# Kernel optimization log

Measured on AMD Instinct MI355X. Metric: run time of the kernel, lower is better.

The kernel has to match this reference:

```python
import jax, jax.numpy as jnp
import numpy as np

DIMS = 1024
STATE = 2 * DIMS
EPS = 1e-8


def _rmsnorm(v, scale):
    # norm = ||v||_2 * d^{-1/2}
    d = v.shape[-1]
    n = jnp.sqrt(jnp.sum(v * v, axis=-1, keepdims=True)) * (d ** -0.5)
    return scale * v / (n + EPS)


def setup_inputs() -> dict:
    key = jax.random.key(0)
    ks = jax.random.split(key, 5)
    x = jax.random.normal(ks[0], (4, 2048, DIMS), dtype=jnp.float32)
    ls_scale = jnp.ones((DIMS // 2,), dtype=jnp.float32)
    rs_scale = jnp.ones((DIMS // 2,), dtype=jnp.float32)
    split_scale = jnp.full((DIMS,), 0.1, dtype=jnp.float32)
    sk = (1.0 / DIMS) ** 0.5
    Wk = jax.random.uniform(ks[1], (DIMS, STATE), jnp.float32, -sk, sk)
    Wugg = jax.random.uniform(ks[2], (DIMS, 3 * STATE), jnp.float32, -sk, sk)
    so = (1.0 / STATE) ** 0.5
    Wout = jax.random.uniform(ks[3], (STATE, DIMS), jnp.float32, -so, so)
    return {"x": x, "ls_scale": ls_scale, "rs_scale": rs_scale,
            "split_scale": split_scale, "Wk": Wk, "Wugg": Wugg, "Wout": Wout}


def reference(x, ls_scale, rs_scale, split_scale, Wk, Wugg, Wout):
    residual = x
    # RMS_split norm (output_dim=None)
    xl, xr = jnp.split(x, 2, axis=-1)
    xn = jnp.concatenate([_rmsnorm(xl, ls_scale), _rmsnorm(xr, rs_scale)], axis=-1)
    xn = xn * split_scale

    K = jax.nn.sigmoid(xn @ Wk)                      # [B,S,STATE]
    u, g_in, g_out = jnp.split(xn @ Wugg, 3, axis=-1)
    u = u * jax.nn.sigmoid(g_in) * (1.0 - K)

    # linear recurrence: h_0 = u_0; h_t = K_{t-1} * h_{t-1} + u_t
    a = jnp.concatenate([jnp.ones_like(K[..., :1, :]), K[..., :-1, :]], axis=-2)

    def combine(lhs, rhs):
        aL, bL = lhs
        aR, bR = rhs
        return (aL * aR, bL * aR + bR)

    _, h = jax.lax.associative_scan(combine, (a, u), axis=1)
    outputs = h * jax.nn.sigmoid(g_out)
    y = outputs @ Wout
    return y + residual
```

## Files before the change

### kernel.cpp

```cpp
#include <hip/hip_runtime.h>
#include <hip/hip_bf16.h>
#include <hip/hip_fp8.h>
#include <stdint.h>

#define DIMS 1024
#define STATE 2048
#define BATCH 4
#define SEQ 2048
#define TOKENS 8192
#define N1 8192
#define NCHUNK 16
#define CHUNKL (SEQ / NCHUNK)

typedef __hip_bfloat16 bf16;
typedef unsigned char u8;
typedef unsigned short u16;
typedef __attribute__((ext_vector_type(8))) short bf16x8;
typedef __attribute__((ext_vector_type(4))) float f32x4;
typedef __attribute__((ext_vector_type(16))) float f32x16;
typedef __attribute__((ext_vector_type(2))) long v2i64;

#define XN_SCALE 32.0f
#define W1_SCALE 256.0f
#define INV_SCALE (1.0f / 8192.0f)

__device__ __forceinline__ float sigmoidf_(float x) {
  return 1.0f / (1.0f + __expf(-x));
}

__device__ __forceinline__ u8 to_fp8(float f) {
  __hip_fp8_e4m3 h(f);
  return h.__x;
}

__device__ __forceinline__ float b2f(u16 v) {
  union { uint32_t u; float f; } w;
  w.u = ((uint32_t)v) << 16;
  return w.f;
}

__device__ __forceinline__ int kperm(int k) {
  return (k & ~24) | ((k & 8) << 1) | ((k & 16) >> 1);
}

__device__ __forceinline__ void async_copy16(const void* g, void* l) {
  __builtin_amdgcn_global_load_lds(
      (const __attribute__((address_space(1))) void*)(uintptr_t)g,
      (__attribute__((address_space(3))) void*)(uint32_t)(uintptr_t)l,
      16, 0, 0);
}

__device__ __forceinline__ int swz32(int row, int kc) {
  int line = row >> 1;
  int sub = ((row & 1) << 2) | kc;
  return (line << 3) | (sub ^ (line & 7));
}
__device__ __forceinline__ void swz32_dec(int c, int& row, int& kc) {
  int line = c >> 3;
  int sub = (c & 7) ^ (line & 7);
  row = (line << 1) | (sub >> 2);
  kc = sub & 3;
}
__device__ __forceinline__ int swz64(int row, int kc) {
  return (row << 3) | (kc ^ (row & 7));
}
__device__ __forceinline__ void swz64_dec(int c, int& row, int& kc) {
  row = c >> 3;
  kc = (c & 7) ^ (row & 7);
}

__global__ __launch_bounds__(256) void transpose_bf16_kernel(
    const float* __restrict__ W, bf16* __restrict__ Wt, int K, int N) {
  __shared__ float tile[32][33];
  int tx = threadIdx.x & 31;
  int ty = threadIdx.x >> 5;
  long col = (long)blockIdx.x * 32 + tx;
  long rowb = (long)blockIdx.y * 32;
#pragma unroll
  for (int i = 0; i < 32; i += 8)
    tile[ty + i][tx] = W[(rowb + ty + i) * N + col];
  __syncthreads();
  long ocol = rowb + tx;
  long orow = (long)blockIdx.x * 32 + ty;
#pragma unroll
  for (int i = 0; i < 32; i += 8)
    Wt[(orow + i) * K + ocol] = __float2bfloat16(tile[tx][ty + i]);
}

__global__ __launch_bounds__(256) void transpose_fp8_kernel(
    const float* __restrict__ W, u8* __restrict__ Wt, int K, int N, int stream_base) {
  __shared__ float tile[32][33];
  int tx = threadIdx.x & 31;
  int ty = threadIdx.x >> 5;
  long col = (long)blockIdx.x * 32 + tx;
  long rowb = (long)blockIdx.y * 32;
#pragma unroll
  for (int i = 0; i < 32; i += 8)
    tile[ty + i][tx] = W[(rowb + ty + i) * N + col];
  __syncthreads();
  long ocol = rowb + kperm(tx);
  long orow = (long)blockIdx.x * 32 + ty;
#pragma unroll
  for (int i = 0; i < 32; i += 8) {
    long n = orow + i;
    long dstrow = ((n & 2047) << 2) | (stream_base + (n >> 11));
    Wt[dstrow * K + ocol] = to_fp8(tile[tx][ty + i] * W1_SCALE);
  }
}

__global__ __launch_bounds__(256) void rmsnorm_kernel(
    const float* __restrict__ x, const float* __restrict__ ls,
    const float* __restrict__ rs, const float* __restrict__ ss,
    u8* __restrict__ xn8) {
  int token = blockIdx.x;
  int tid = threadIdx.x;
  const float4* xt = (const float4*)(x + (long)token * DIMS);
  float4 v = xt[tid];
  float s = v.x * v.x + v.y * v.y + v.z * v.z + v.w * v.w;
#pragma unroll
  for (int d = 32; d > 0; d >>= 1) s += __shfl_down(s, d);
  __shared__ float parts[4];
  if ((tid & 63) == 0) parts[tid >> 6] = s;
  __syncthreads();
  int j = tid * 4;
  bool left = j < 512;
  float sum = left ? (parts[0] + parts[1]) : (parts[2] + parts[3]);
  float n = sqrtf(sum * (1.0f / 512.0f));
  float inv = 1.0f / (n + 1e-8f);
  const float4* sc = (const float4*)(left ? ls : rs);
  float4 g = sc[left ? tid : tid - 128];
  float4 p = ((const float4*)ss)[tid];
  u8 q[4];
  q[0] = to_fp8(v.x * g.x * inv * p.x * XN_SCALE);
  q[1] = to_fp8(v.y * g.y * inv * p.y * XN_SCALE);
  q[2] = to_fp8(v.z * g.z * inv * p.z * XN_SCALE);
  q[3] = to_fp8(v.w * g.w * inv * p.w * XN_SCALE);
  *(uint32_t*)(xn8 + (long)token * DIMS + kperm(j)) = *(uint32_t*)q;
}

__device__ __forceinline__ void g1f8_stage(const u8* __restrict__ A,
                                           const u8* __restrict__ Bt,
                                           long arow0, long brow0, int k0,
                                           int wave, int lane, u8* As, u8* Bs) {
  const int K = DIMS;
#pragma unroll
  for (int i = 0; i < 4; i++) {
    int c = (wave * 4 + i) * 64 + lane;
    int row, kc; swz32_dec(c, row, kc);
    async_copy16(A + (arow0 + row) * K + k0 + kc * 16, (char*)As + (wave * 4 + i) * 1024);
  }
#pragma unroll
  for (int i = 0; i < 2; i++) {
    int c = (wave * 2 + i) * 64 + lane;
    int row, kc; swz32_dec(c, row, kc);
    async_copy16(Bt + (brow0 + row) * K + k0 + kc * 16, (char*)Bs + (wave * 2 + i) * 1024);
  }
}

__global__ __launch_bounds__(256, 2) void gemm1_fp8(
    const u8* __restrict__ A, const u8* __restrict__ Bt, bf16* __restrict__ C) {
  __shared__ __align__(16) u8 As0[256 * 64], As1[256 * 64];
  __shared__ __align__(16) u8 Bs0[128 * 64], Bs1[128 * 64];
  int tid = threadIdx.x;
  int lane = tid & 63, wave = tid >> 6;
  int wm = wave & 1, wn = wave >> 1;
  long arow0 = (long)blockIdx.y * 256;
  long brow0 = (long)blockIdx.x * 128;
  int m_lane = lane & 31, q4 = lane >> 5;
  f32x16 acc[4][2] = {};

  g1f8_stage(A, Bt, arow0, brow0, 0, wave, lane, As0, Bs0);
  __syncthreads();

  for (int it = 0; it < 16; it += 2) {
    {
      v2i64 af[2][4], bfr[2][2];
#pragma unroll
      for (int p = 0; p < 2; p++) {
#pragma unroll
        for (int mt = 0; mt < 4; mt++)
          af[p][mt] = *(const v2i64*)(As0 + swz32(wm * 128 + mt * 32 + m_lane, p * 2 + q4) * 16);
#pragma unroll
        for (int nt = 0; nt < 2; nt++)
          bfr[p][nt] = *(const v2i64*)(Bs0 + swz32(wn * 64 + nt * 32 + m_lane, p * 2 + q4) * 16);
      }
      g1f8_stage(A, Bt, arow0, brow0, (it + 1) * 64, wave, lane, As1, Bs1);
#pragma unroll
      for (int p = 0; p < 2; p++)
#pragma unroll
        for (int mt = 0; mt < 4; mt++)
#pragma unroll
          for (int nt = 0; nt < 2; nt++) {
            acc[mt][nt] = __builtin_amdgcn_mfma_f32_32x32x16_fp8_fp8(bfr[p][nt][0], af[p][mt][0], acc[mt][nt], 0, 0, 0);
            acc[mt][nt] = __builtin_amdgcn_mfma_f32_32x32x16_fp8_fp8(bfr[p][nt][1], af[p][mt][1], acc[mt][nt], 0, 0, 0);
          }
      __syncthreads();
    }
    {
      v2i64 af[2][4], bfr[2][2];
#pragma unroll
      for (int p = 0; p < 2; p++) {
#pragma unroll
        for (int mt = 0; mt < 4; mt++)
          af[p][mt] = *(const v2i64*)(As1 + swz32(wm * 128 + mt * 32 + m_lane, p * 2 + q4) * 16);
#pragma unroll
        for (int nt = 0; nt < 2; nt++)
          bfr[p][nt] = *(const v2i64*)(Bs1 + swz32(wn * 64 + nt * 32 + m_lane, p * 2 + q4) * 16);
      }
      if (it + 2 < 16)
        g1f8_stage(A, Bt, arow0, brow0, (it + 2) * 64, wave, lane, As0, Bs0);
#pragma unroll
      for (int p = 0; p < 2; p++)
#pragma unroll
        for (int mt = 0; mt < 4; mt++)
#pragma unroll
          for (int nt = 0; nt < 2; nt++) {
            acc[mt][nt] = __builtin_amdgcn_mfma_f32_32x32x16_fp8_fp8(bfr[p][nt][0], af[p][mt][0], acc[mt][nt], 0, 0, 0);
            acc[mt][nt] = __builtin_amdgcn_mfma_f32_32x32x16_fp8_fp8(bfr[p][nt][1], af[p][mt][1], acc[mt][nt], 0, 0, 0);
          }
      __syncthreads();
    }
  }
#pragma unroll
  for (int mt = 0; mt < 4; mt++) {
    long row = arow0 + wm * 128 + mt * 32 + m_lane;
#pragma unroll
    for (int nt = 0; nt < 2; nt++) {
#pragma unroll
      for (int g = 0; g < 4; g++) {
        long col = brow0 + wn * 64 + nt * 32 + g * 8 + q4 * 4;
        bf16 tmp[4];
#pragma unroll
        for (int j = 0; j < 4; j++)
          tmp[j] = __float2bfloat16(acc[mt][nt][g * 4 + j] * INV_SCALE);
        *(uint2*)(C + row * N1 + col) = *(uint2*)tmp;
      }
    }
  }
}

__device__ __forceinline__ void g2_stage(const bf16* __restrict__ A,
                                         const bf16* __restrict__ Bt,
                                         long arow0, long brow0, int k0, int K,
                                         int wave, int lane, bf16* As, bf16* Bs) {
#pragma unroll
  for (int i = 0; i < 4; i++) {
    int c = (wave * 4 + i) * 64 + lane;
    int row, kc; swz64_dec(c, row, kc);
    async_copy16(A + (arow0 + row) * K + k0 + kc * 8, (char*)As + (wave * 4 + i) * 1024);
    async_copy16(Bt + (brow0 + row) * K + k0 + kc * 8, (char*)Bs + (wave * 4 + i) * 1024);
  }
}

__global__ __launch_bounds__(256) void gemm2_resid(
    const bf16* __restrict__ A, const bf16* __restrict__ Bt,
    float* __restrict__ C, const float* __restrict__ resid) {
  __shared__ __align__(16) bf16 As0[128 * 64], As1[128 * 64];
  __shared__ __align__(16) bf16 Bs0[128 * 64], Bs1[128 * 64];
  const int K = STATE, N = DIMS;
  int tid = threadIdx.x;
  int lane = tid & 63, wave = tid >> 6;
  int wm = wave & 1, wn = wave >> 1;
  long arow0 = (long)blockIdx.y * 128;
  long brow0 = (long)blockIdx.x * 128;
  int r = lane & 15, q = lane >> 4;
  f32x4 acc[4][4] = {};

  g2_stage(A, Bt, arow0, brow0, 0, K, wave, lane, As0, Bs0);
  __syncthreads();

  for (int it = 0; it < 32; it += 2) {
    {
      const bf16x8* AsV = (const bf16x8*)As0;
      const bf16x8* BsV = (const bf16x8*)Bs0;
      bf16x8 af[2][4], bfr[2][4];
#pragma unroll
      for (int ks = 0; ks < 2; ks++) {
#pragma unroll
        for (int mt = 0; mt < 4; mt++) af[ks][mt] = AsV[swz64(wm * 64 + mt * 16 + r, ks * 4 + q)];
#pragma unroll
        for (int nt = 0; nt < 4; nt++) bfr[ks][nt] = BsV[swz64(wn * 64 + nt * 16 + r, ks * 4 + q)];
      }
      g2_stage(A, Bt, arow0, brow0, (it + 1) * 64, K, wave, lane, As1, Bs1);
#pragma unroll
      for (int ks = 0; ks < 2; ks++)
#pragma unroll
        for (int mt = 0; mt < 4; mt++)
#pragma unroll
          for (int nt = 0; nt < 4; nt++)
            acc[mt][nt] = __builtin_amdgcn_mfma_f32_16x16x32_bf16(bfr[ks][nt], af[ks][mt], acc[mt][nt], 0, 0, 0);
      __syncthreads();
    }
    {
      const bf16x8* AsV = (const bf16x8*)As1;
      const bf16x8* BsV = (const bf16x8*)Bs1;
      bf16x8 af[2][4], bfr[2][4];
#pragma unroll
      for (int ks = 0; ks < 2; ks++) {
#pragma unroll
        for (int mt = 0; mt < 4; mt++) af[ks][mt] = AsV[swz64(wm * 64 + mt * 16 + r, ks * 4 + q)];
#pragma unroll
        for (int nt = 0; nt < 4; nt++) bfr[ks][nt] = BsV[swz64(wn * 64 + nt * 16 + r, ks * 4 + q)];
      }
      if (it + 2 < 32)
        g2_stage(A, Bt, arow0, brow0, (it + 2) * 64, K, wave, lane, As0, Bs0);
#pragma unroll
      for (int ks = 0; ks < 2; ks++)
#pragma unroll
        for (int mt = 0; mt < 4; mt++)
#pragma unroll
          for (int nt = 0; nt < 4; nt++)
            acc[mt][nt] = __builtin_amdgcn_mfma_f32_16x16x32_bf16(bfr[ks][nt], af[ks][mt], acc[mt][nt], 0, 0, 0);
      __syncthreads();
    }
  }

#pragma unroll
  for (int mt = 0; mt < 4; mt++) {
    long row = arow0 + wm * 64 + mt * 16 + r;
#pragma unroll
    for (int nt = 0; nt < 4; nt++) {
      long col = brow0 + wn * 64 + nt * 16 + q * 4;
      float4 rv = *(const float4*)(resid + row * N + col);
      float4 ov;
      ov.x = acc[mt][nt][0] + rv.x;
      ov.y = acc[mt][nt][1] + rv.y;
      ov.z = acc[mt][nt][2] + rv.z;
      ov.w = acc[mt][nt][3] + rv.w;
      *(float4*)(C + row * N + col) = ov;
    }
  }
}


__global__ __launch_bounds__(256) void chunk_summary_kernel(
    const bf16* __restrict__ C1, float* __restrict__ carryA,
    float* __restrict__ carryU) {
  int b = blockIdx.x;
  int ch = blockIdx.y * 256 + threadIdx.x;
  int chunk = blockIdx.z;
  int t0 = chunk * CHUNKL;
  const bf16* base = C1 + ((long)b * SEQ) * N1 + ch * 4;
  float kp = 0.0f;
  if (chunk != 0) kp = __bfloat162float(base[(long)(t0 - 1) * N1]);
  float a_first = (chunk == 0) ? 1.0f : sigmoidf_(kp);
  float A = 1.0f, U = 0.0f;
#pragma unroll 8
  for (int t = t0; t < t0 + CHUNKL; t++) {
    union { uint2 u2; u16 h[4]; } w;
    w.u2 = *(const uint2*)(base + (long)t * N1);
    float kraw = b2f(w.h[0]);
    float uraw = b2f(w.h[1]);
    float gin  = b2f(w.h[2]);
    float a = (t == t0) ? a_first : sigmoidf_(kp);
    float sK = sigmoidf_(kraw);
    float u = uraw * sigmoidf_(gin) * (1.0f - sK);
    A *= a;
    U = a * U + u;
    kp = kraw;
  }
  int cidx = (b * NCHUNK + chunk) * STATE + ch;
  carryA[cidx] = A;
  carryU[cidx] = U;
}

__global__ __launch_bounds__(256) void carry_scan_kernel(
    const float* __restrict__ carryA, const float* __restrict__ carryU,
    float* __restrict__ carryIn) {
  int idx = blockIdx.x * 256 + threadIdx.x;
  int b = idx >> 11;
  int ch = idx & 2047;
  float h = 0.0f;
#pragma unroll
  for (int c = 0; c < NCHUNK; c++) {
    int cidx = (b * NCHUNK + c) * STATE + ch;
    carryIn[cidx] = h;
    h = carryA[cidx] * h + carryU[cidx];
  }
}

__global__ __launch_bounds__(256) void scan_chunk_kernel(
    const bf16* __restrict__ C1, const float* __restrict__ carryIn,
    bf16* __restrict__ out) {
  int b = blockIdx.x;
  int c0 = blockIdx.y * 32;
  int chunk = blockIdx.z;
  int tstart = chunk * CHUNKL;
  __shared__ float a_s[32][65], u_s[32][65], h_s[32][65];
  int tid = threadIdx.x;
  int lane = tid & 63, wave = tid >> 6;
  int cc = tid & 31;
  int tq = tid >> 5;

  float carryH[8], carryK[8];
#pragma unroll
  for (int i = 0; i < 8; i++) {
    int ch = c0 + wave * 8 + i;
    carryH[i] = carryIn[(b * NCHUNK + chunk) * STATE + ch];
    carryK[i] = (chunk == 0)
                    ? 1.0f
                    : sigmoidf_(__bfloat162float(
                          C1[((long)(b * SEQ + tstart - 1)) * N1 + ch * 4]));
  }

  float g_r[8];
  for (int t0 = tstart; t0 < tstart + CHUNKL; t0 += 64) {
#pragma unroll
    for (int i = 0; i < 8; i++) {
      int t = tq * 8 + i;
      union { uint2 u2; u16 h[4]; } w;
      w.u2 = *(const uint2*)(C1 + ((long)(b * SEQ + t0 + t)) * N1 + (c0 + cc) * 4);
      float kraw = b2f(w.h[0]);
      float uraw = b2f(w.h[1]);
      float gin  = b2f(w.h[2]);
      float gout = b2f(w.h[3]);
      float aK = sigmoidf_(kraw);
      a_s[cc][t] = aK;
      u_s[cc][t] = uraw * sigmoidf_(gin) * (1.0f - aK);
      g_r[i] = sigmoidf_(gout);
    }
    __syncthreads();
#pragma unroll
    for (int i = 0; i < 8; i++) {
      int ch = wave * 8 + i;
      float aK = a_s[ch][lane];
      float u = u_s[ch][lane];
      float a = __shfl_up(aK, 1);
      if (lane == 0) a = carryK[i];
      float A = a, U = u;
#pragma unroll
      for (int d = 1; d < 64; d <<= 1) {
        float Au = __shfl_up(A, d);
        float Uu = __shfl_up(U, d);
        if (lane >= d) { U += A * Uu; A *= Au; }
      }
      float h = U + A * carryH[i];
      carryH[i] = __shfl(h, 63);
      carryK[i] = __shfl(aK, 63);
      h_s[ch][lane] = h;
    }
    __syncthreads();
#pragma unroll
    for (int i = 0; i < 8; i++) {
      int t = tq * 8 + i;
      out[((long)(b * SEQ + t0 + t)) * STATE + c0 + cc] =
          __float2bfloat16(h_s[cc][t] * g_r[i]);
    }
    __syncthreads();
  }
}

extern "C" void kernel_launch(void* const* d_in, const int* in_sizes, int n_in,
                              void* d_out, int out_size, void* d_ws, size_t ws_size,
                              hipStream_t stream) {
  const float* x    = (const float*)d_in[0];
  const float* ls   = (const float*)d_in[1];
  const float* rs   = (const float*)d_in[2];
  const float* ss   = (const float*)d_in[3];
  const float* Wk   = (const float*)d_in[4];
  const float* Wugg = (const float*)d_in[5];
  const float* Wout = (const float*)d_in[6];
  float* out = (float*)d_out;

  char* ws = (char*)d_ws;
  u8*   W1f8 = (u8*)ws;
  bf16* W2t  = (bf16*)(ws + 8388608);
  u8*   xn8  = (u8*)(ws + 8388608 + 4194304);
  bf16* C1   = (bf16*)(ws + 8388608 + 4194304 + 8388608);
  bf16* sco  = (bf16*)(ws + 8388608 + 4194304 + 8388608 + 134217728);
  float* carryA  = (float*)xn8;
  float* carryU  = carryA + BATCH * NCHUNK * STATE;
  float* carryIn = carryU + BATCH * NCHUNK * STATE;

  transpose_fp8_kernel<<<dim3(STATE / 32, DIMS / 32), 256, 0, stream>>>(
      Wk, W1f8, DIMS, STATE, 0);
  transpose_fp8_kernel<<<dim3(3 * STATE / 32, DIMS / 32), 256, 0, stream>>>(
      Wugg, W1f8, DIMS, 3 * STATE, 1);
  transpose_bf16_kernel<<<dim3(DIMS / 32, STATE / 32), 256, 0, stream>>>(Wout, W2t, STATE, DIMS);

  rmsnorm_kernel<<<TOKENS, 256, 0, stream>>>(x, ls, rs, ss, xn8);

  gemm1_fp8<<<dim3(N1 / 128, TOKENS / 256), 256, 0, stream>>>(xn8, W1f8, C1);

  chunk_summary_kernel<<<dim3(BATCH, STATE / 256, NCHUNK), 256, 0, stream>>>(
      C1, carryA, carryU);
  carry_scan_kernel<<<dim3(BATCH * STATE / 256), 256, 0, stream>>>(
      carryA, carryU, carryIn);
  scan_chunk_kernel<<<dim3(BATCH, STATE / 32, NCHUNK), 256, 0, stream>>>(
      C1, carryIn, sco);

  gemm2_resid<<<dim3(DIMS / 128, TOKENS / 128), 256, 0, stream>>>(
      sco, W2t, out, x);
}
```

Baseline: 387.3 us.

## Fuse gate sigmoids into GEMM1 epilogue, emit packed (a,u) and gate tensors

Moves the sigmoid and gating math out of the scan kernels into the GEMM1 epilogue. GEMM1 now writes a packed bf16 pair (sigmoid(K), u) as one 32-bit word per channel plus a separate bf16 sigmoid(g_out) array, instead of four raw bf16 projections. The summary kernel reads only the packed word, dropping the g_out bytes and the repeated sigmoid work. The total intermediate size stays about the same, but the scan kernels now issue narrower loads from differently strided arrays, and the epilogue stores become 4-byte and 2-byte scattered writes.

```diff
diff --git a/kernel.cpp b/kernel.cpp
--- a/kernel.cpp
+++ b/kernel.cpp
@@ -37,6 +37,11 @@
   union { uint32_t u; float f; } w;
   w.u = ((uint32_t)v) << 16;
   return w.f;
+}
+__device__ __forceinline__ u16 f2bb(float f) {
+  union { bf16 b; u16 u; } v;
+  v.b = __float2bfloat16(f);
+  return v.u;
 }
 
 __device__ __forceinline__ int kperm(int k) {
@@ -158,7 +163,8 @@
 }
 
 __global__ __launch_bounds__(256, 2) void gemm1_fp8(
-    const u8* __restrict__ A, const u8* __restrict__ Bt, bf16* __restrict__ C) {
+    const u8* __restrict__ A, const u8* __restrict__ Bt,
+    uint32_t* __restrict__ P, bf16* __restrict__ G) {
   __shared__ __align__(16) u8 As0[256 * 64], As1[256 * 64];
   __shared__ __align__(16) u8 Bs0[128 * 64], Bs1[128 * 64];
   int tid = threadIdx.x;
@@ -228,12 +234,16 @@
     for (int nt = 0; nt < 2; nt++) {
 #pragma unroll
       for (int g = 0; g < 4; g++) {
-        long col = brow0 + wn * 64 + nt * 32 + g * 8 + q4 * 4;
-        bf16 tmp[4];
-#pragma unroll
-        for (int j = 0; j < 4; j++)
-          tmp[j] = __float2bfloat16(acc[mt][nt][g * 4 + j] * INV_SCALE);
-        *(uint2*)(C + row * N1 + col) = *(uint2*)tmp;
+        long ch = (brow0 >> 2) + wn * 16 + nt * 8 + g * 2 + q4;
+        float kraw = acc[mt][nt][g * 4 + 0] * INV_SCALE;
+        float uraw = acc[mt][nt][g * 4 + 1] * INV_SCALE;
+        float gin  = acc[mt][nt][g * 4 + 2] * INV_SCALE;
+        float gout = acc[mt][nt][g * 4 + 3] * INV_SCALE;
+        float aK = sigmoidf_(kraw);
+        float u  = uraw * sigmoidf_(gin) * (1.0f - aK);
+        float gg = sigmoidf_(gout);
+        P[row * STATE + ch] = (uint32_t)f2bb(aK) | ((uint32_t)f2bb(u) << 16);
+        G[row * STATE + ch] = __float2bfloat16(gg);
       }
     }
   }
@@ -334,30 +344,24 @@
 
 
 __global__ __launch_bounds__(256) void chunk_summary_kernel(
-    const bf16* __restrict__ C1, float* __restrict__ carryA,
+    const uint32_t* __restrict__ P, float* __restrict__ carryA,
     float* __restrict__ carryU) {
   int b = blockIdx.x;
   int ch = blockIdx.y * 256 + threadIdx.x;
   int chunk = blockIdx.z;
   int t0 = chunk * CHUNKL;
-  const bf16* base = C1 + ((long)b * SEQ) * N1 + ch * 4;
-  float kp = 0.0f;
-  if (chunk != 0) kp = __bfloat162float(base[(long)(t0 - 1) * N1]);
-  float a_first = (chunk == 0) ? 1.0f : sigmoidf_(kp);
+  const uint32_t* base = P + ((long)b * SEQ) * STATE + ch;
+  float a_carry = 1.0f;
+  if (chunk != 0) a_carry = b2f((u16)(base[(long)(t0 - 1) * STATE] & 0xffff));
   float A = 1.0f, U = 0.0f;
 #pragma unroll 8
   for (int t = t0; t < t0 + CHUNKL; t++) {
-    union { uint2 u2; u16 h[4]; } w;
-    w.u2 = *(const uint2*)(base + (long)t * N1);
-    float kraw = b2f(w.h[0]);
-    float uraw = b2f(w.h[1]);
-    float gin  = b2f(w.h[2]);
-    float a = (t == t0) ? a_first : sigmoidf_(kp);
-    float sK = sigmoidf_(kraw);
-    float u = uraw * sigmoidf_(gin) * (1.0f - sK);
-    A *= a;
-    U = a * U + u;
-    kp = kraw;
+    uint32_t w = base[(long)t * STATE];
+    float aK = b2f((u16)(w & 0xffff));
+    float u  = b2f((u16)(w >> 16));
+    A *= a_carry;
+    U = a_carry * U + u;
+    a_carry = aK;
   }
   int cidx = (b * NCHUNK + chunk) * STATE + ch;
   carryA[cidx] = A;
@@ -380,8 +384,8 @@
 }
 
 __global__ __launch_bounds__(256) void scan_chunk_kernel(
-    const bf16* __restrict__ C1, const float* __restrict__ carryIn,
-    bf16* __restrict__ out) {
+    const uint32_t* __restrict__ P, const bf16* __restrict__ G,
+    const float* __restrict__ carryIn, bf16* __restrict__ out) {
   int b = blockIdx.x;
   int c0 = blockIdx.y * 32;
   int chunk = blockIdx.z;
@@ -399,8 +403,7 @@
     carryH[i] = carryIn[(b * NCHUNK + chunk) * STATE + ch];
     carryK[i] = (chunk == 0)
                     ? 1.0f
-                    : sigmoidf_(__bfloat162float(
-                          C1[((long)(b * SEQ + tstart - 1)) * N1 + ch * 4]));
+                    : b2f((u16)(P[((long)(b * SEQ + tstart - 1)) * STATE + ch] & 0xffff));
   }
 
   float g_r[8];
@@ -408,16 +411,11 @@
 #pragma unroll
     for (int i = 0; i < 8; i++) {
       int t = tq * 8 + i;
-      union { uint2 u2; u16 h[4]; } w;
-      w.u2 = *(const uint2*)(C1 + ((long)(b * SEQ + t0 + t)) * N1 + (c0 + cc) * 4);
-      float kraw = b2f(w.h[0]);
-      float uraw = b2f(w.h[1]);
-      float gin  = b2f(w.h[2]);
-      float gout = b2f(w.h[3]);
-      float aK = sigmoidf_(kraw);
-      a_s[cc][t] = aK;
-      u_s[cc][t] = uraw * sigmoidf_(gin) * (1.0f - aK);
-      g_r[i] = sigmoidf_(gout);
+      long idx = ((long)(b * SEQ + t0 + t)) * STATE + c0 + cc;
+      uint32_t w = P[idx];
+      a_s[cc][t] = b2f((u16)(w & 0xffff));
+      u_s[cc][t] = b2f((u16)(w >> 16));
+      g_r[i] = __bfloat162float(G[idx]);
     }
     __syncthreads();
 #pragma unroll
@@ -463,11 +461,12 @@
   float* out = (float*)d_out;
 
   char* ws = (char*)d_ws;
-  u8*   W1f8 = (u8*)ws;
-  bf16* W2t  = (bf16*)(ws + 8388608);
-  u8*   xn8  = (u8*)(ws + 8388608 + 4194304);
-  bf16* C1   = (bf16*)(ws + 8388608 + 4194304 + 8388608);
-  bf16* sco  = (bf16*)(ws + 8388608 + 4194304 + 8388608 + 134217728);
+  u8*       W1f8 = (u8*)ws;
+  bf16*     W2t  = (bf16*)(ws + 8388608);
+  u8*       xn8  = (u8*)(ws + 8388608 + 4194304);
+  uint32_t* P    = (uint32_t*)(ws + 20971520);
+  bf16*     G    = (bf16*)(ws + 20971520 + 67108864);
+  bf16*     sco  = (bf16*)(ws + 20971520 + 67108864 + 33554432);
   float* carryA  = (float*)xn8;
   float* carryU  = carryA + BATCH * NCHUNK * STATE;
   float* carryIn = carryU + BATCH * NCHUNK * STATE;
@@ -480,14 +479,14 @@
 
   rmsnorm_kernel<<<TOKENS, 256, 0, stream>>>(x, ls, rs, ss, xn8);
 
-  gemm1_fp8<<<dim3(N1 / 128, TOKENS / 256), 256, 0, stream>>>(xn8, W1f8, C1);
+  gemm1_fp8<<<dim3(N1 / 128, TOKENS / 256), 256, 0, stream>>>(xn8, W1f8, P, G);
 
   chunk_summary_kernel<<<dim3(BATCH, STATE / 256, NCHUNK), 256, 0, stream>>>(
-      C1, carryA, carryU);
+      P, carryA, carryU);
   carry_scan_kernel<<<dim3(BATCH * STATE / 256), 256, 0, stream>>>(
       carryA, carryU, carryIn);
   scan_chunk_kernel<<<dim3(BATCH, STATE / 32, NCHUNK), 256, 0, stream>>>(
-      C1, carryIn, sco);
+      P, G, carryIn, sco);
 
   gemm2_resid<<<dim3(DIMS / 128, TOKENS / 128), 256, 0, stream>>>(
       sco, W2t, out, x);
```

Result: slower. 405.0 us (+4.6%).

## Switch output GEMM to FP8 with scaled scan output and FP8 transposed weights

Applied to the files above, without the earlier changes.

Converts the second GEMM (scan outputs times Wout) from bf16 to fp8 e4m3. The scan kernel now writes fp8 with a fixed scale and k-permuted columns, and the weight transpose emits fp8. The GEMM uses 32x32x16 fp8 MFMAs and rescales in the epilogue. This halves the operand bytes and raises MFMA throughput, at the cost of accuracy risk from fixed-scale fp8 quantization of activations and weights.

```diff
diff --git a/kernel.cpp b/kernel.cpp
--- a/kernel.cpp
+++ b/kernel.cpp
@@ -15,13 +15,14 @@
 typedef __hip_bfloat16 bf16;
 typedef unsigned char u8;
 typedef unsigned short u16;
-typedef __attribute__((ext_vector_type(8))) short bf16x8;
 typedef __attribute__((ext_vector_type(4))) float f32x4;
 typedef __attribute__((ext_vector_type(16))) float f32x16;
 typedef __attribute__((ext_vector_type(2))) long v2i64;
 
 #define XN_SCALE 32.0f
 #define W1_SCALE 256.0f
+#define H_SCALE  32.0f
+#define W2_SCALE 256.0f
 #define INV_SCALE (1.0f / 8192.0f)
 
 __device__ __forceinline__ float sigmoidf_(float x) {
@@ -61,16 +62,10 @@
   row = (line << 1) | (sub >> 2);
   kc = sub & 3;
 }
-__device__ __forceinline__ int swz64(int row, int kc) {
-  return (row << 3) | (kc ^ (row & 7));
-}
-__device__ __forceinline__ void swz64_dec(int c, int& row, int& kc) {
-  row = c >> 3;
-  kc = (c & 7) ^ (row & 7);
-}
-
-__global__ __launch_bounds__(256) void transpose_bf16_kernel(
-    const float* __restrict__ W, bf16* __restrict__ Wt, int K, int N) {
+
+__global__ __launch_bounds__(256) void transpose_fp8_kernel(
+    const float* __restrict__ W, u8* __restrict__ Wt, int K, int N,
+    int stream_base, int interleave, float scale) {
   __shared__ float tile[32][33];
   int tx = threadIdx.x & 31;
   int ty = threadIdx.x >> 5;
@@ -80,31 +75,13 @@
   for (int i = 0; i < 32; i += 8)
     tile[ty + i][tx] = W[(rowb + ty + i) * N + col];
   __syncthreads();
-  long ocol = rowb + tx;
-  long orow = (long)blockIdx.x * 32 + ty;
-#pragma unroll
-  for (int i = 0; i < 32; i += 8)
-    Wt[(orow + i) * K + ocol] = __float2bfloat16(tile[tx][ty + i]);
-}
-
-__global__ __launch_bounds__(256) void transpose_fp8_kernel(
-    const float* __restrict__ W, u8* __restrict__ Wt, int K, int N, int stream_base) {
-  __shared__ float tile[32][33];
-  int tx = threadIdx.x & 31;
-  int ty = threadIdx.x >> 5;
-  long col = (long)blockIdx.x * 32 + tx;
-  long rowb = (long)blockIdx.y * 32;
-#pragma unroll
-  for (int i = 0; i < 32; i += 8)
-    tile[ty + i][tx] = W[(rowb + ty + i) * N + col];
-  __syncthreads();
   long ocol = rowb + kperm(tx);
   long orow = (long)blockIdx.x * 32 + ty;
 #pragma unroll
   for (int i = 0; i < 32; i += 8) {
     long n = orow + i;
-    long dstrow = ((n & 2047) << 2) | (stream_base + (n >> 11));
-    Wt[dstrow * K + ocol] = to_fp8(tile[tx][ty + i] * W1_SCALE);
+    long dstrow = interleave ? (((n & 2047) << 2) | (stream_base + (n >> 11))) : n;
+    Wt[dstrow * K + ocol] = to_fp8(tile[tx][ty + i] * scale);
   }
 }
 
@@ -239,99 +216,109 @@
   }
 }
 
-__device__ __forceinline__ void g2_stage(const bf16* __restrict__ A,
-                                         const bf16* __restrict__ Bt,
-                                         long arow0, long brow0, int k0, int K,
-                                         int wave, int lane, bf16* As, bf16* Bs) {
-#pragma unroll
-  for (int i = 0; i < 4; i++) {
-    int c = (wave * 4 + i) * 64 + lane;
-    int row, kc; swz64_dec(c, row, kc);
-    async_copy16(A + (arow0 + row) * K + k0 + kc * 8, (char*)As + (wave * 4 + i) * 1024);
-    async_copy16(Bt + (brow0 + row) * K + k0 + kc * 8, (char*)Bs + (wave * 4 + i) * 1024);
-  }
-}
-
-__global__ __launch_bounds__(256) void gemm2_resid(
-    const bf16* __restrict__ A, const bf16* __restrict__ Bt,
+__device__ __forceinline__ void g2f8_stage(const u8* __restrict__ A,
+                                           const u8* __restrict__ Bt,
+                                           long arow0, long brow0, int k0,
+                                           int wave, int lane, u8* As, u8* Bs) {
+  const int K = STATE;
+#pragma unroll
+  for (int i = 0; i < 2; i++) {
+    int c = (wave * 2 + i) * 64 + lane;
+    int row, kc; swz32_dec(c, row, kc);
+    async_copy16(A + (arow0 + row) * K + k0 + kc * 16, (char*)As + (wave * 2 + i) * 1024);
+  }
+#pragma unroll
+  for (int i = 0; i < 2; i++) {
+    int c = (wave * 2 + i) * 64 + lane;
+    int row, kc; swz32_dec(c, row, kc);
+    async_copy16(Bt + (brow0 + row) * K + k0 + kc * 16, (char*)Bs + (wave * 2 + i) * 1024);
+  }
+}
+
+__global__ __launch_bounds__(256) void gemm2_fp8(
+    const u8* __restrict__ A, const u8* __restrict__ Bt,
     float* __restrict__ C, const float* __restrict__ resid) {
-  __shared__ __align__(16) bf16 As0[128 * 64], As1[128 * 64];
-  __shared__ __align__(16) bf16 Bs0[128 * 64], Bs1[128 * 64];
-  const int K = STATE, N = DIMS;
+  __shared__ __align__(16) u8 As0[128 * 64], As1[128 * 64];
+  __shared__ __align__(16) u8 Bs0[128 * 64], Bs1[128 * 64];
   int tid = threadIdx.x;
   int lane = tid & 63, wave = tid >> 6;
   int wm = wave & 1, wn = wave >> 1;
   long arow0 = (long)blockIdx.y * 128;
   long brow0 = (long)blockIdx.x * 128;
-  int r = lane & 15, q = lane >> 4;
-  f32x4 acc[4][4] = {};
-
-  g2_stage(A, Bt, arow0, brow0, 0, K, wave, lane, As0, Bs0);
+  int m_lane = lane & 31, q4 = lane >> 5;
+  f32x16 acc[2][2] = {};
+
+  g2f8_stage(A, Bt, arow0, brow0, 0, wave, lane, As0, Bs0);
   __syncthreads();
 
   for (int it = 0; it < 32; it += 2) {
     {
-      const bf16x8* AsV = (const bf16x8*)As0;
-      const bf16x8* BsV = (const bf16x8*)Bs0;
-      bf16x8 af[2][4], bfr[2][4];
-#pragma unroll
-      for (int ks = 0; ks < 2; ks++) {
-#pragma unroll
-        for (int mt = 0; mt < 4; mt++) af[ks][mt] = AsV[swz64(wm * 64 + mt * 16 + r, ks * 4 + q)];
-#pragma unroll
-        for (int nt = 0; nt < 4; nt++) bfr[ks][nt] = BsV[swz64(wn * 64 + nt * 16 + r, ks * 4 + q)];
-      }
-      g2_stage(A, Bt, arow0, brow0, (it + 1) * 64, K, wave, lane, As1, Bs1);
-#pragma unroll
-      for (int ks = 0; ks < 2; ks++)
-#pragma unroll
-        for (int mt = 0; mt < 4; mt++)
-#pragma unroll
-          for (int nt = 0; nt < 4; nt++)
-            acc[mt][nt] = __builtin_amdgcn_mfma_f32_16x16x32_bf16(bfr[ks][nt], af[ks][mt], acc[mt][nt], 0, 0, 0);
+      v2i64 af[2][2], bfr[2][2];
+#pragma unroll
+      for (int p = 0; p < 2; p++) {
+#pragma unroll
+        for (int mt = 0; mt < 2; mt++)
+          af[p][mt] = *(const v2i64*)(As0 + swz32(wm * 64 + mt * 32 + m_lane, p * 2 + q4) * 16);
+#pragma unroll
+        for (int nt = 0; nt < 2; nt++)
+          bfr[p][nt] = *(const v2i64*)(Bs0 + swz32(wn * 64 + nt * 32 + m_lane, p * 2 + q4) * 16);
+      }
+      g2f8_stage(A, Bt, arow0, brow0, (it + 1) * 64, wave, lane, As1, Bs1);
+#pragma unroll
+      for (int p = 0; p < 2; p++)
+#pragma unroll
+        for (int mt = 0; mt < 2; mt++)
+#pragma unroll
+          for (int nt = 0; nt < 2; nt++) {
+            acc[mt][nt] = __builtin_amdgcn_mfma_f32_32x32x16_fp8_fp8(bfr[p][nt][0], af[p][mt][0], acc[mt][nt], 0, 0, 0);
+            acc[mt][nt] = __builtin_amdgcn_mfma_f32_32x32x16_fp8_fp8(bfr[p][nt][1], af[p][mt][1], acc[mt][nt], 0, 0, 0);
+          }
       __syncthreads();
     }
     {
-      const bf16x8* AsV = (const bf16x8*)As1;
-      const bf16x8* BsV = (const bf16x8*)Bs1;
-      bf16x8 af[2][4], bfr[2][4];
-#pragma unroll
-      for (int ks = 0; ks < 2; ks++) {
-#pragma unroll
-        for (int mt = 0; mt < 4; mt++) af[ks][mt] = AsV[swz64(wm * 64 + mt * 16 + r, ks * 4 + q)];
-#pragma unroll
-        for (int nt = 0; nt < 4; nt++) bfr[ks][nt] = BsV[swz64(wn * 64 + nt * 16 + r, ks * 4 + q)];
+      v2i64 af[2][2], bfr[2][2];
+#pragma unroll
+      for (int p = 0; p < 2; p++) {
+#pragma unroll
+        for (int mt = 0; mt < 2; mt++)
+          af[p][mt] = *(const v2i64*)(As1 + swz32(wm * 64 + mt * 32 + m_lane, p * 2 + q4) * 16);
+#pragma unroll
+        for (int nt = 0; nt < 2; nt++)
+          bfr[p][nt] = *(const v2i64*)(Bs1 + swz32(wn * 64 + nt * 32 + m_lane, p * 2 + q4) * 16);
       }
       if (it + 2 < 32)
-        g2_stage(A, Bt, arow0, brow0, (it + 2) * 64, K, wave, lane, As0, Bs0);
-#pragma unroll
-      for (int ks = 0; ks < 2; ks++)
-#pragma unroll
-        for (int mt = 0; mt < 4; mt++)
-#pragma unroll
-          for (int nt = 0; nt < 4; nt++)
-            acc[mt][nt] = __builtin_amdgcn_mfma_f32_16x16x32_bf16(bfr[ks][nt], af[ks][mt], acc[mt][nt], 0, 0, 0);
+        g2f8_stage(A, Bt, arow0, brow0, (it + 2) * 64, wave, lane, As0, Bs0);
+#pragma unroll
+      for (int p = 0; p < 2; p++)
+#pragma unroll
+        for (int mt = 0; mt < 2; mt++)
+#pragma unroll
+          for (int nt = 0; nt < 2; nt++) {
+            acc[mt][nt] = __builtin_amdgcn_mfma_f32_32x32x16_fp8_fp8(bfr[p][nt][0], af[p][mt][0], acc[mt][nt], 0, 0, 0);
+            acc[mt][nt] = __builtin_amdgcn_mfma_f32_32x32x16_fp8_fp8(bfr[p][nt][1], af[p][mt][1], acc[mt][nt], 0, 0, 0);
+          }
       __syncthreads();
     }
   }
-
-#pragma unroll
-  for (int mt = 0; mt < 4; mt++) {
-    long row = arow0 + wm * 64 + mt * 16 + r;
-#pragma unroll
-    for (int nt = 0; nt < 4; nt++) {
-      long col = brow0 + wn * 64 + nt * 16 + q * 4;
-      float4 rv = *(const float4*)(resid + row * N + col);
-      float4 ov;
-      ov.x = acc[mt][nt][0] + rv.x;
-      ov.y = acc[mt][nt][1] + rv.y;
-      ov.z = acc[mt][nt][2] + rv.z;
-      ov.w = acc[mt][nt][3] + rv.w;
-      *(float4*)(C + row * N + col) = ov;
-    }
-  }
-}
-
+#pragma unroll
+  for (int mt = 0; mt < 2; mt++) {
+    long row = arow0 + wm * 64 + mt * 32 + m_lane;
+#pragma unroll
+    for (int nt = 0; nt < 2; nt++) {
+#pragma unroll
+      for (int g = 0; g < 4; g++) {
+        long col = brow0 + wn * 64 + nt * 32 + g * 8 + q4 * 4;
+        float4 rv = *(const float4*)(resid + row * DIMS + col);
+        float4 ov;
+        ov.x = acc[mt][nt][g * 4 + 0] * INV_SCALE + rv.x;
+        ov.y = acc[mt][nt][g * 4 + 1] * INV_SCALE + rv.y;
+        ov.z = acc[mt][nt][g * 4 + 2] * INV_SCALE + rv.z;
+        ov.w = acc[mt][nt][g * 4 + 3] * INV_SCALE + rv.w;
+        *(float4*)(C + row * DIMS + col) = ov;
+      }
+    }
+  }
+}
 
 __global__ __launch_bounds__(256) void chunk_summary_kernel(
     const bf16* __restrict__ C1, float* __restrict__ carryA,
@@ -381,7 +368,7 @@
 
 __global__ __launch_bounds__(256) void scan_chunk_kernel(
     const bf16* __restrict__ C1, const float* __restrict__ carryIn,
-    bf16* __restrict__ out) {
+    u8* __restrict__ sco8) {
   int b = blockIdx.x;
   int c0 = blockIdx.y * 32;
   int chunk = blockIdx.z;
@@ -443,8 +430,8 @@
 #pragma unroll
     for (int i = 0; i < 8; i++) {
       int t = tq * 8 + i;
-      out[((long)(b * SEQ + t0 + t)) * STATE + c0 + cc] =
-          __float2bfloat16(h_s[cc][t] * g_r[i]);
+      sco8[((long)(b * SEQ + t0 + t)) * STATE + c0 + kperm(cc)] =
+          to_fp8(h_s[cc][t] * g_r[i] * H_SCALE);
     }
     __syncthreads();
   }
@@ -464,19 +451,20 @@
 
   char* ws = (char*)d_ws;
   u8*   W1f8 = (u8*)ws;
-  bf16* W2t  = (bf16*)(ws + 8388608);
-  u8*   xn8  = (u8*)(ws + 8388608 + 4194304);
-  bf16* C1   = (bf16*)(ws + 8388608 + 4194304 + 8388608);
-  bf16* sco  = (bf16*)(ws + 8388608 + 4194304 + 8388608 + 134217728);
+  u8*   W2f8 = (u8*)(ws + 8388608);
+  u8*   xn8  = (u8*)(ws + 8388608 + 2097152);
+  bf16* C1   = (bf16*)(ws + 18874368);
+  u8*   sco8 = (u8*)(ws + 18874368 + 134217728);
   float* carryA  = (float*)xn8;
   float* carryU  = carryA + BATCH * NCHUNK * STATE;
   float* carryIn = carryU + BATCH * NCHUNK * STATE;
 
   transpose_fp8_kernel<<<dim3(STATE / 32, DIMS / 32), 256, 0, stream>>>(
-      Wk, W1f8, DIMS, STATE, 0);
+      Wk, W1f8, DIMS, STATE, 0, 1, W1_SCALE);
   transpose_fp8_kernel<<<dim3(3 * STATE / 32, DIMS / 32), 256, 0, stream>>>(
-      Wugg, W1f8, DIMS, 3 * STATE, 1);
-  transpose_bf16_kernel<<<dim3(DIMS / 32, STATE / 32), 256, 0, stream>>>(Wout, W2t, STATE, DIMS);
+      Wugg, W1f8, DIMS, 3 * STATE, 1, 1, W1_SCALE);
+  transpose_fp8_kernel<<<dim3(DIMS / 32, STATE / 32), 256, 0, stream>>>(
+      Wout, W2f8, STATE, DIMS, 0, 0, W2_SCALE);
 
   rmsnorm_kernel<<<TOKENS, 256, 0, stream>>>(x, ls, rs, ss, xn8);
 
@@ -487,8 +475,8 @@
   carry_scan_kernel<<<dim3(BATCH * STATE / 256), 256, 0, stream>>>(
       carryA, carryU, carryIn);
   scan_chunk_kernel<<<dim3(BATCH, STATE / 32, NCHUNK), 256, 0, stream>>>(
-      C1, carryIn, sco);
-
-  gemm2_resid<<<dim3(DIMS / 128, TOKENS / 128), 256, 0, stream>>>(
-      sco, W2t, out, x);
-}
+      C1, carryIn, sco8);
+
+  gemm2_fp8<<<dim3(DIMS / 128, TOKENS / 128), 256, 0, stream>>>(
+      sco8, W2f8, out, x);
+}
```

Result: no change. 384.7 us (-0.7%).
